# Performance work log

Hardware: AMD Instinct MI355X
Metric: run time of the kernel (lower is better)

Reference implementation:

```python
import jax, jax.numpy as jnp
import numpy as np

S = 0.7071067811865476  # 1/sqrt(2), haar filter coefficient


def wavelet_kernels():
    # pywt haar: dec_lo=[s,s], dec_hi=[-s,s], rec_lo=[s,s], rec_hi=[s,-s]
    # module reverses dec filters -> dec_lo_rev=[s,s], dec_hi_rev=[s,-s]
    lo_d = jnp.array([S, S], jnp.float32)
    hi_d = jnp.array([S, -S], jnp.float32)
    lo_r = jnp.array([S, S], jnp.float32)
    hi_r = jnp.array([S, -S], jnp.float32)
    # torch builds k[i,j] = row_filter[i] * col_filter[j] with (row, col) = (2nd, 1st) unsqueeze
    Kd = jnp.stack([jnp.outer(lo_d, lo_d), jnp.outer(hi_d, lo_d),
                    jnp.outer(lo_d, hi_d), jnp.outer(hi_d, hi_d)])  # [4,2,2] LL,LH,HL,HH
    Kr = 4.0 * jnp.stack([jnp.outer(lo_r, lo_r), jnp.outer(hi_r, lo_r),
                          jnp.outer(lo_r, hi_r), jnp.outer(hi_r, hi_r)])  # rec_* * 4
    return Kd, Kr


def group_norm(x, gamma, beta, groups, eps=1e-5):
    B, C, H, W = x.shape
    xg = x.reshape(B, groups, C // groups, H, W)
    mu = xg.mean(axis=(2, 3, 4), keepdims=True)
    var = xg.var(axis=(2, 3, 4), keepdims=True)
    xn = ((xg - mu) * jax.lax.rsqrt(var + eps)).reshape(B, C, H, W)
    return xn * gamma[None, :, None, None] + beta[None, :, None, None]


def conv2d(x, w, b, stride=1, pad=1):
    y = jax.lax.conv_general_dilated(x, w, (stride, stride), [(pad, pad), (pad, pad)],
                                     dimension_numbers=('NCHW', 'OIHW', 'NCHW'))
    return y + b[None, :, None, None]


def conv_transpose2d(x, w, b, stride=2, pad=1):
    # w in torch layout [Cin, Cout, kh, kw]; transpose conv == conv with
    # lhs-dilated input, spatially flipped kernel, padding k-1-pad
    wf = jnp.flip(w, (-2, -1)).transpose(1, 0, 2, 3)
    p = w.shape[-1] - 1 - pad
    y = jax.lax.conv_general_dilated(x, wf, (1, 1), [(p, p), (p, p)],
                                     lhs_dilation=(stride, stride),
                                     dimension_numbers=('NCHW', 'OIHW', 'NCHW'))
    return y + b[None, :, None, None]


def dwt2d(x, Kd):
    # haar k=2, stride=2, pad=0 -> non-overlapping 2x2 blocks; exact conv2d equivalent
    B, C, H, W = x.shape
    xr = x.reshape(B, C, H // 2, 2, W // 2, 2)
    c = jnp.einsum('bchdwe,sde->bcshw', xr, Kd)  # s in {LL,LH,HL,HH}
    return c.reshape(B, C * 4, H // 2, W // 2)   # channel layout [c0:LL,LH,HL,HH, c1:...]


def idwt2d(c, Kr):
    # conv_transpose2d k=2, stride=2, pad=0 -> pure 2x2 interleave
    B, C4, Hh, Wh = c.shape
    C = C4 // 4
    cr = c.reshape(B, C, 4, Hh, Wh)
    y = jnp.einsum('bcshw,sde->bchdwe', cr, Kr)
    return y.reshape(B, C, 2 * Hh, 2 * Wh)


def _forward(x, Kd, Kr, W1, b1, g1, be1, W2, b2, g2, be2, W3, b3, g3, be3,
             W4, b4, g4, be4, Wt, bt, g5, be5, W6, b6):
    h = dwt2d(x, Kd)                                      # [B,32,H/2,W/2]
    h = jax.nn.relu(group_norm(conv2d(h, W1, b1, 1, 1), g1, be1, 8))    # 32->64
    h = jax.nn.relu(group_norm(conv2d(h, W2, b2, 2, 1), g2, be2, 16))   # 64->128, /2
    h = jax.nn.relu(group_norm(conv2d(h, W3, b3, 1, 1), g3, be3, 32))   # 128->256
    h = jax.nn.relu(group_norm(conv2d(h, W4, b4, 1, 1), g4, be4, 16))   # 256->128
    h = jax.nn.relu(group_norm(conv_transpose2d(h, Wt, bt, 2, 1), g5, be5, 8))  # 128->64, x2
    h = conv2d(h, W6, b6, 1, 1)                            # 64->16
    return idwt2d(h, Kr)                                   # [B,4,H,W]


def setup_inputs() -> dict:
    key = jax.random.key(0)
    ks = jax.random.split(key, 16)
    B, Cin, H, W = 16, 8, 256, 256
    bc = 64
    Kd, Kr = wavelet_kernels()
    w = lambda k, s: jax.random.normal(k, s, jnp.float32) * 0.05
    return {
        'x': jax.random.normal(ks[0], (B, Cin, H, W), jnp.float32),
        'Kd': Kd, 'Kr': Kr,
        'W1': w(ks[1], (bc, Cin * 4, 3, 3)), 'b1': jnp.zeros(bc),
        'g1': jnp.ones(bc), 'be1': jnp.zeros(bc),
        'W2': w(ks[2], (bc * 2, bc, 3, 3)), 'b2': jnp.zeros(bc * 2),
        'g2': jnp.ones(bc * 2), 'be2': jnp.zeros(bc * 2),
        'W3': w(ks[3], (bc * 4, bc * 2, 3, 3)), 'b3': jnp.zeros(bc * 4),
        'g3': jnp.ones(bc * 4), 'be3': jnp.zeros(bc * 4),
        'W4': w(ks[4], (bc * 2, bc * 4, 3, 3)), 'b4': jnp.zeros(bc * 2),
        'g4': jnp.ones(bc * 2), 'be4': jnp.zeros(bc * 2),
        'Wt': w(ks[5], (bc * 2, bc, 4, 4)), 'bt': jnp.zeros(bc),  # torch convT layout [in,out,kh,kw]
        'g5': jnp.ones(bc), 'be5': jnp.zeros(bc),
        'W6': w(ks[6], (4 * 4, bc, 3, 3)), 'b6': jnp.zeros(4 * 4),
    }


def reference(x, Kd, Kr, W1, b1, g1, be1, W2, b2, g2, be2, W3, b3, g3, be3,
              W4, b4, g4, be4, Wt, bt, g5, be5, W6, b6):
    return _forward(x, Kd, Kr, W1, b1, g1, be1, W2, b2, g2, be2, W3, b3, g3, be3,
                    W4, b4, g4, be4, Wt, bt, g5, be5, W6, b6)
```

## Files before the change

kernel.cpp:

```cpp
#include <hip/hip_runtime.h>

typedef unsigned short ushort_t;
typedef unsigned int uint_t;
typedef __attribute__((ext_vector_type(8))) short short8;
typedef __attribute__((ext_vector_type(4))) float f32x4;

#define PAD 40

__device__ __forceinline__ ushort_t f2bf(float f) {
    uint_t u = __float_as_uint(f);
    u = (u + 0x7FFFu + ((u >> 16) & 1u)) >> 16;
    return (ushort_t)u;
}
__device__ __forceinline__ float bf2f(ushort_t h) {
    return __uint_as_float(((uint_t)h) << 16);
}

__device__ __forceinline__ void red_stats(float& s, float& ss) {
    s += __shfl_xor(s, 16); ss += __shfl_xor(ss, 16);
    s += __shfl_xor(s, 32); ss += __shfl_xor(ss, 32);
    s += __shfl_xor(s, 1);  ss += __shfl_xor(ss, 1);
    s += __shfl_xor(s, 2);  ss += __shfl_xor(ss, 2);
    s += __shfl_xor(s, 4);  ss += __shfl_xor(ss, 4);
}

__device__ __forceinline__ uint4 gn8(uint4 v, const float2* ss) {
    uint_t u[4] = {v.x, v.y, v.z, v.w};
    uint_t r[4];
#pragma unroll
    for (int p = 0; p < 4; ++p) {
        float2 s0 = ss[2 * p], s1 = ss[2 * p + 1];
        float f0 = fmaxf(bf2f((ushort_t)(u[p] & 0xffffu)) * s0.x + s0.y, 0.f);
        float f1 = fmaxf(bf2f((ushort_t)(u[p] >> 16)) * s1.x + s1.y, 0.f);
        r[p] = (uint_t)f2bf(f0) | ((uint_t)f2bf(f1) << 16);
    }
    return make_uint4(r[0], r[1], r[2], r[3]);
}

template<int C, int NPB>
__device__ __forceinline__ void fill_ss(float2* sshare, const float2* __restrict__ pin,
                                        const float* __restrict__ gamma,
                                        const float* __restrict__ beta,
                                        int b, float invC, int tid) {
    for (int c = tid; c < C; c += 256) {
        const float2* p = pin + ((size_t)b * (C / 8) + (c >> 3)) * NPB;
        float s = 0.f, ss = 0.f;
#pragma unroll 8
        for (int i = 0; i < NPB; ++i) { s += p[i].x; ss += p[i].y; }
        float mean = s * invC;
        float rstd = rsqrtf(ss * invC - mean * mean + 1e-5f);
        float sc = gamma[c] * rstd;
        sshare[c] = make_float2(sc, beta[c] - mean * sc);
    }
}

template<int CIN, int COUT>
__device__ __forceinline__ void pack3(const float* __restrict__ W, ushort_t* __restrict__ wp, int idx) {
    int kk = idx & 31;
    int t = idx >> 5;
    int co = t % COUT; t /= COUT;
    int tap = t % 9;
    int cib = t / 9;
    wp[idx] = f2bf(W[(co * CIN + cib * 32 + kk) * 9 + tap]);
}

__device__ __forceinline__ void pack2p(const float* __restrict__ W2, ushort_t* __restrict__ wp, int idx) {
    int kk = idx & 31;
    int co = (idx >> 5) & 127;
    int tap = (idx >> 12) & 3;
    int cib = idx >> 14;
    int p = cib >> 2, q = (cib >> 1) & 1, chalf = cib & 1;
    int kh = 2 * (tap >> 1) + p - 1;
    int kw = 2 * (tap & 1) + q - 1;
    float v = 0.f;
    if (kh >= 0 && kh < 3 && kw >= 0 && kw < 3)
        v = W2[(co * 64 + chalf * 32 + kk) * 9 + kh * 3 + kw];
    wp[idx] = f2bf(v);
}

__device__ __forceinline__ void packt(const float* __restrict__ Wt, ushort_t* __restrict__ wp, int idx) {
    int kk = idx & 31;
    int t = idx >> 5;
    int co = t & 63; t >>= 6;
    int tap = t & 3; t >>= 2;
    int cib = t & 3;
    int ph = t >> 2;
    int rs = tap >> 1, cs = tap & 1;
    int eh = ph >> 1, ew = ph & 1;
    int kh = eh ? (rs ? 0 : 2) : (rs ? 1 : 3);
    int kw = ew ? (cs ? 0 : 2) : (cs ? 1 : 3);
    wp[idx] = f2bf(Wt[((cib * 32 + kk) * 64 + co) * 16 + kh * 4 + kw]);
}

__global__ __launch_bounds__(256) void pack_all(const float* __restrict__ W1,
                                                const float* __restrict__ W2,
                                                const float* __restrict__ W3,
                                                const float* __restrict__ W4,
                                                const float* __restrict__ Wt,
                                                const float* __restrict__ W6,
                                                ushort_t* __restrict__ WP) {
    int idx = blockIdx.x * 256 + threadIdx.x;
    if (idx < 18432)        pack3<32, 64>(W1, WP, idx);
    else if (idx < 149504)  pack2p(W2, WP + 18432, idx - 18432);
    else if (idx < 444416)  pack3<128, 256>(W3, WP + 149504, idx - 149504);
    else if (idx < 739328)  pack3<256, 128>(W4, WP + 444416, idx - 444416);
    else if (idx < 870400)  packt(Wt, WP + 739328, idx - 739328);
    else if (idx < 879616)  pack3<64, 16>(W6, WP + 870400, idx - 870400);
}

__global__ __launch_bounds__(256) void dwt_nhwc(const float* __restrict__ x,
                                                const float* __restrict__ Kd,
                                                ushort_t* __restrict__ out) {
    int idx = blockIdx.x * 256 + threadIdx.x;
    int w = idx & 127, h = (idx >> 7) & 127, b = idx >> 14;
    float k[16];
#pragma unroll
    for (int i = 0; i < 16; ++i) k[i] = Kd[i];
    const float* xb = x + (size_t)b * 8 * 65536;
    uint_t uu[16];
#pragma unroll
    for (int ci = 0; ci < 8; ++ci) {
        const float* p = xb + ci * 65536 + (2 * h) * 256 + 2 * w;
        float2 r0 = *(const float2*)p;
        float2 r1 = *(const float2*)(p + 256);
        ushort_t o[4];
#pragma unroll
        for (int sb = 0; sb < 4; ++sb) {
            float v = r0.x * k[sb*4] + r0.y * k[sb*4+1] + r1.x * k[sb*4+2] + r1.y * k[sb*4+3];
            o[sb] = f2bf(v);
        }
        uu[ci*2]   = (uint_t)o[0] | ((uint_t)o[1] << 16);
        uu[ci*2+1] = (uint_t)o[2] | ((uint_t)o[3] << 16);
    }
    uint4* dst = (uint4*)(out + (size_t)idx * 32);
    dst[0] = make_uint4(uu[0], uu[1], uu[2], uu[3]);
    dst[1] = make_uint4(uu[4], uu[5], uu[6], uu[7]);
    dst[2] = make_uint4(uu[8], uu[9], uu[10], uu[11]);
    dst[3] = make_uint4(uu[12], uu[13], uu[14], uu[15]);
}

__global__ __launch_bounds__(256) void idwt_nhwc(const ushort_t* __restrict__ cin,
                                                 const float* __restrict__ Kr,
                                                 float* __restrict__ out) {
    int idx = blockIdx.x * 256 + threadIdx.x;
    int w = idx & 127, h = (idx >> 7) & 127, b = idx >> 14;
    float k[16];
#pragma unroll
    for (int i = 0; i < 16; ++i) k[i] = Kr[i];
    const uint4* pv = (const uint4*)(cin + (size_t)idx * 16);
    uint4 v0 = pv[0], v1 = pv[1];
    uint_t uw[8] = {v0.x, v0.y, v0.z, v0.w, v1.x, v1.y, v1.z, v1.w};
    float cs[16];
#pragma unroll
    for (int i = 0; i < 8; ++i) {
        cs[2*i]   = bf2f((ushort_t)(uw[i] & 0xffffu));
        cs[2*i+1] = bf2f((ushort_t)(uw[i] >> 16));
    }
#pragma unroll
    for (int c = 0; c < 4; ++c) {
        float y00 = 0, y01 = 0, y10 = 0, y11 = 0;
#pragma unroll
        for (int sb = 0; sb < 4; ++sb) {
            float v = cs[c * 4 + sb];
            y00 += v * k[sb*4];   y01 += v * k[sb*4+1];
            y10 += v * k[sb*4+2]; y11 += v * k[sb*4+3];
        }
        float* ob = out + ((size_t)(b * 4 + c) * 256 + 2 * h) * 256 + 2 * w;
        *(float2*)ob = make_float2(y00, y01);
        *(float2*)(ob + 256) = make_float2(y10, y11);
    }
}

template<int CIN, int COUT, int H, int W, bool STATS, bool GNIN, int NPBI>
__global__ __launch_bounds__(256, 2) void conv_mfma(const ushort_t* __restrict__ in,
                                                    const ushort_t* __restrict__ wp,
                                                    const float* __restrict__ bias,
                                                    ushort_t* __restrict__ outp,
                                                    float2* __restrict__ pstats_out,
                                                    const float2* __restrict__ pstats_in,
                                                    const float* __restrict__ gamma,
                                                    const float* __restrict__ beta,
                                                    float invC) {
    constexpr int NT = (COUT < 64) ? COUT : 64;
    constexpr int NF = NT / 16;
    constexpr int NCB = CIN / 32;
    constexpr int CSTR = (CIN < 64) ? CIN : 64;
    constexpr int NBI = CIN / CSTR;
    constexpr int SUB = CSTR / 32;
    constexpr int NBO = COUT / NT;
    constexpr int IW = 66, NRI = 6;
    constexpr int AITER = NRI * IW * 4;
    constexpr int CA = (AITER + 255) / 256;
    constexpr int NW = W / 64, NH = H / 4;
    constexpr int PB = NBO * NW * NH;
    constexpr int NPBO = NH * NW;
    constexpr int EP = NT + 8;
    constexpr int ASZ = NRI * IW * PAD;
    constexpr int SMEM = (ASZ > 256 * EP) ? ASZ : 256 * EP;

    __shared__ ushort_t smem[SMEM];
    __shared__ float2 sred[4][8];
    __shared__ float2 sshare[CIN];
    ushort_t* lA = smem;
    ushort_t* lE = smem;

    int bid = blockIdx.x;
    int xcd = bid & 7;
    int rest = bid >> 3;
    int half = rest / PB;
    int local = rest - half * PB;
    int b = xcd + 8 * half;
    int ht = local % NH; local /= NH;
    int wt = local % NW; local /= NW;
    int nb = local;
    int h0 = ht * 4, w0 = wt * 64, n0 = nb * NT;
    int tid = threadIdx.x;
    int lane = tid & 63, wid = tid >> 6;
    int nl = lane & 15, quad = lane >> 4, ql = quad * 8;

    if (GNIN) {
        fill_ss<CIN, NPBI>(sshare, pstats_in, gamma, beta, b, invC, tid);
        __syncthreads();
    }

    int ga[CA], la[CA], pr[CA];
#pragma unroll
    for (int r = 0; r < CA; ++r) {
        int i = tid + r * 256;
        ga[r] = -1; la[r] = 0; pr[r] = 0;
        if (i < AITER) {
            int tr = i / (IW * 4); int rem = i - tr * (IW * 4);
            int p = rem >> 2, part = rem & 3;
            la[r] = (tr * IW + p) * PAD + part * 8;
            pr[r] = part;
            int ih = h0 - 1 + tr, iw = w0 - 1 + p;
            if ((unsigned)ih < (unsigned)H && (unsigned)iw < (unsigned)W)
                ga[r] = (ih * W + iw) * CSTR + part * 8;
        }
    }

    f32x4 acc[4][NF];
#pragma unroll
    for (int mf = 0; mf < 4; ++mf)
#pragma unroll
        for (int nf = 0; nf < NF; ++nf)
            acc[mf][nf] = (f32x4){0.f, 0.f, 0.f, 0.f};

    uint4 ra[CA];

    auto loadA = [&](int cib) {
        const int blk = cib / SUB;
        const int inner = (cib - blk * SUB) * 32;
        const ushort_t* base = in + ((size_t)(b * NBI + blk) * (H * W)) * CSTR + inner;
#pragma unroll
        for (int r = 0; r < CA; ++r) {
            uint4 v = make_uint4(0, 0, 0, 0);
            if (ga[r] >= 0) {
                v = *(const uint4*)(base + ga[r]);
                if (GNIN) v = gn8(v, &sshare[cib * 32 + pr[r] * 8]);
            }
            ra[r] = v;
        }
    };

    loadA(0);

    const ushort_t* wlane = wp + ((size_t)(n0 + nl)) * 32 + ql;

    for (int cib = 0; cib < NCB; ++cib) {
        __syncthreads();
#pragma unroll
        for (int r = 0; r < CA; ++r)
            if (tid + r * 256 < AITER) *(uint4*)&lA[la[r]] = ra[r];
        __syncthreads();
        if (cib + 1 < NCB) loadA(cib + 1);

        const ushort_t* wc = wlane + (size_t)cib * 9 * COUT * 32;
        short8 bfc[NF], bfn[NF];
#pragma unroll
        for (int nf = 0; nf < NF; ++nf)
            bfc[nf] = *(const short8*)(wc + nf * 512);

#pragma unroll
        for (int tap = 0; tap < 9; ++tap) {
            const int kh = tap / 3, kw = tap % 3;
            if (tap < 8) {
#pragma unroll
                for (int nf = 0; nf < NF; ++nf)
                    bfn[nf] = *(const short8*)(wc + (size_t)(tap + 1) * COUT * 32 + nf * 512);
            }
            short8 af[4];
#pragma unroll
            for (int mf = 0; mf < 4; ++mf)
                af[mf] = *(const short8*)&lA[((wid + kh) * IW + mf * 16 + nl + kw) * PAD + ql];
#pragma unroll
            for (int mf = 0; mf < 4; ++mf)
#pragma unroll
                for (int nf = 0; nf < NF; ++nf)
                    acc[mf][nf] = __builtin_amdgcn_mfma_f32_16x16x32_bf16(
                        af[mf], bfc[nf], acc[mf][nf], 0, 0, 0);
#pragma unroll
            for (int nf = 0; nf < NF; ++nf) bfc[nf] = bfn[nf];
        }
    }

    float bs[NF];
#pragma unroll
    for (int nf = 0; nf < NF; ++nf) bs[nf] = bias[n0 + nf * 16 + nl];

    if (STATS) {
#pragma unroll
        for (int nf = 0; nf < NF; ++nf) {
            float s = 0.f, ss = 0.f;
#pragma unroll
            for (int mf = 0; mf < 4; ++mf)
#pragma unroll
                for (int rg = 0; rg < 4; ++rg) {
                    float v = acc[mf][nf][rg] + bs[nf];
                    s += v; ss += v * v;
                }
            red_stats(s, ss);
            if (quad == 0 && (nl & 7) == 0) sred[wid][nf * 2 + (nl >> 3)] = make_float2(s, ss);
        }
    }

    __syncthreads();
#pragma unroll
    for (int mf = 0; mf < 4; ++mf)
#pragma unroll
        for (int nf = 0; nf < NF; ++nf)
#pragma unroll
            for (int rg = 0; rg < 4; ++rg) {
                int px = wid * 64 + mf * 16 + quad * 4 + rg;
                lE[px * EP + nf * 16 + nl] = f2bf(acc[mf][nf][rg] + bs[nf]);
            }
    __syncthreads();
#pragma unroll
    for (int it = 0; it < NT / 8; ++it) {
        int idx = it * 256 + tid;
        int px = idx / (NT / 8), ck = idx % (NT / 8);
        int row = px >> 6, col = px & 63;
        uint4 v = *(const uint4*)&lE[px * EP + ck * 8];
        *(uint4*)(outp + ((((size_t)(b * NBO + nb) * H + h0 + row) * W + w0 + col) * NT + ck * 8)) = v;
    }
    if (STATS && tid < 2 * NF) {
        float2 t0 = sred[0][tid], t1 = sred[1][tid], t2 = sred[2][tid], t3 = sred[3][tid];
        pstats_out[((size_t)b * (COUT / 8) + (n0 >> 3) + tid) * NPBO + (ht * NW + wt)] =
            make_float2(t0.x + t1.x + t2.x + t3.x, t0.y + t1.y + t2.y + t3.y);
    }
}

__global__ __launch_bounds__(256, 2) void conv2p_mfma(const ushort_t* __restrict__ in,
                                                      const ushort_t* __restrict__ wp,
                                                      const float* __restrict__ bias,
                                                      ushort_t* __restrict__ outp,
                                                      float2* __restrict__ pstats_out,
                                                      const float2* __restrict__ pstats_in,
                                                      const float* __restrict__ gamma,
                                                      const float* __restrict__ beta,
                                                      float invC) {
    constexpr int IW = 65, NRI = 5, NF = 4, NT = 64;
    constexpr int AITER = NRI * IW * 4;
    constexpr int CA = 6;
    constexpr int EP = NT + 8;
    constexpr int ASZ = NRI * IW * PAD;
    constexpr int SMEM = (ASZ > 256 * EP) ? ASZ : 256 * EP;
    __shared__ ushort_t smem[SMEM];
    __shared__ float2 sred[4][8];
    __shared__ float2 sshare[64];
    ushort_t* lA = smem;
    ushort_t* lE = smem;

    int bid = blockIdx.x;
    int xcd = bid & 7;
    int rest = bid >> 3;
    int half = rest >> 5;
    int local = rest & 31;
    int b = xcd + 8 * half;
    int ht = local & 15;
    int nb = local >> 4;
    int h0 = ht * 4, n0 = nb * 64;
    int tid = threadIdx.x;
    int lane = tid & 63, wid = tid >> 6;
    int nl = lane & 15, quad = lane >> 4, ql = quad * 8;

    fill_ss<64, 64>(sshare, pstats_in, gamma, beta, b, invC, tid);
    __syncthreads();

    int r2[CA], c2[CA], la[CA], g4[CA], pr[CA];
#pragma unroll
    for (int r = 0; r < CA; ++r) {
        int i = tid + r * 256;
        r2[r] = -1000; c2[r] = 0; la[r] = 0; g4[r] = 0; pr[r] = 0;
        if (i < AITER) {
            int tr = i / (IW * 4); int rem = i - tr * (IW * 4);
            int p = rem >> 2, part = rem & 3;
            r2[r] = 2 * (h0 - 1 + tr);
            c2[r] = 2 * (p - 1);
            la[r] = (tr * IW + p) * PAD + part * 8;
            g4[r] = part * 8;
            pr[r] = part;
        }
    }

    f32x4 acc[4][NF];
#pragma unroll
    for (int mf = 0; mf < 4; ++mf)
#pragma unroll
        for (int nf = 0; nf < NF; ++nf)
            acc[mf][nf] = (f32x4){0.f, 0.f, 0.f, 0.f};

    const ushort_t* ibase = in + (size_t)b * 128 * 128 * 64;
    uint4 ra[CA];

    auto loadA = [&](int cib) {
        const int p = cib >> 2, q = (cib >> 1) & 1, ch32 = (cib & 1) * 32;
#pragma unroll
        for (int r = 0; r < CA; ++r) {
            int ih = r2[r] + p, iw = c2[r] + q;
            uint4 v = make_uint4(0, 0, 0, 0);
            if ((unsigned)ih < 128u && (unsigned)iw < 128u) {
                v = *(const uint4*)(ibase + ((ih << 7) + iw) * 64 + ch32 + g4[r]);
                v = gn8(v, &sshare[ch32 + pr[r] * 8]);
            }
            ra[r] = v;
        }
    };

    loadA(0);
    const ushort_t* wlane = wp + ((size_t)(n0 + nl)) * 32 + ql;

#pragma unroll
    for (int cib = 0; cib < 8; ++cib) {
        const int p = cib >> 2, q = (cib >> 1) & 1;
        __syncthreads();
#pragma unroll
        for (int r = 0; r < CA; ++r)
            if (tid + r * 256 < AITER) *(uint4*)&lA[la[r]] = ra[r];
        __syncthreads();
        if (cib + 1 < 8) loadA(cib + 1);

        const ushort_t* wc = wlane + (size_t)cib * 4 * 128 * 32;
#pragma unroll
        for (int kh = 0; kh < 2; ++kh)
#pragma unroll
            for (int kw = 0; kw < 2; ++kw)
                if ((kh == 1 || p == 1) && (kw == 1 || q == 1)) {
                    const int tap = kh * 2 + kw;
                    short8 bf[NF];
#pragma unroll
                    for (int nf = 0; nf < NF; ++nf)
                        bf[nf] = *(const short8*)(wc + (size_t)tap * 128 * 32 + nf * 512);
                    short8 af[4];
#pragma unroll
                    for (int mf = 0; mf < 4; ++mf)
                        af[mf] = *(const short8*)&lA[((wid + kh) * IW + mf * 16 + nl + kw) * PAD + ql];
#pragma unroll
                    for (int mf = 0; mf < 4; ++mf)
#pragma unroll
                        for (int nf = 0; nf < NF; ++nf)
                            acc[mf][nf] = __builtin_amdgcn_mfma_f32_16x16x32_bf16(
                                af[mf], bf[nf], acc[mf][nf], 0, 0, 0);
                }
    }

    float bs[NF];
#pragma unroll
    for (int nf = 0; nf < NF; ++nf) bs[nf] = bias[n0 + nf * 16 + nl];
#pragma unroll
    for (int nf = 0; nf < NF; ++nf) {
        float s = 0.f, ss = 0.f;
#pragma unroll
        for (int mf = 0; mf < 4; ++mf)
#pragma unroll
            for (int rg = 0; rg < 4; ++rg) {
                float v = acc[mf][nf][rg] + bs[nf];
                s += v; ss += v * v;
            }
        red_stats(s, ss);
        if (quad == 0 && (nl & 7) == 0) sred[wid][nf * 2 + (nl >> 3)] = make_float2(s, ss);
    }

    __syncthreads();
#pragma unroll
    for (int mf = 0; mf < 4; ++mf)
#pragma unroll
        for (int nf = 0; nf < NF; ++nf)
#pragma unroll
            for (int rg = 0; rg < 4; ++rg) {
                int px = wid * 64 + mf * 16 + quad * 4 + rg;
                lE[px * EP + nf * 16 + nl] = f2bf(acc[mf][nf][rg] + bs[nf]);
            }
    __syncthreads();
#pragma unroll
    for (int it = 0; it < 8; ++it) {
        int idx = it * 256 + tid;
        int px = idx >> 3, ck = idx & 7;
        int row = px >> 6, col = px & 63;
        uint4 v = *(const uint4*)&lE[px * EP + ck * 8];
        *(uint4*)(outp + ((((size_t)(b * 2 + nb) * 64 + h0 + row) * 64 + col) * 64 + ck * 8)) = v;
    }
    if (tid < 8) {
        float2 t0 = sred[0][tid], t1 = sred[1][tid], t2 = sred[2][tid], t3 = sred[3][tid];
        pstats_out[((size_t)b * 16 + (n0 >> 3) + tid) * 16 + ht] =
            make_float2(t0.x + t1.x + t2.x + t3.x, t0.y + t1.y + t2.y + t3.y);
    }
}

__global__ __launch_bounds__(256, 2) void convt_mfma(const ushort_t* __restrict__ in,
                                                     const ushort_t* __restrict__ wp,
                                                     const float* __restrict__ bias,
                                                     ushort_t* __restrict__ outp,
                                                     float2* __restrict__ pstats_out,
                                                     const float2* __restrict__ pstats_in,
                                                     const float* __restrict__ gamma,
                                                     const float* __restrict__ beta,
                                                     float invC) {
    constexpr int CIN = 128, COUT = 64, NT = 64, NF = 4;
    constexpr int IW = 66, NRI = 5;
    constexpr int AITER = NRI * IW * 4;
    constexpr int CA = 6;
    constexpr int EP = NT + 8;
    constexpr int ASZ = NRI * IW * PAD;
    constexpr int SMEM = (ASZ > 256 * EP) ? ASZ : 256 * EP;
    __shared__ ushort_t smem[SMEM];
    __shared__ float2 sred[4][8];
    __shared__ float2 sshare[CIN];
    ushort_t* lA = smem;
    ushort_t* lE = smem;

    int bid = blockIdx.x;
    int xcd = bid & 7;
    int rest = bid >> 3;
    int half = rest >> 6;
    int local = rest & 63;
    int b = xcd + 8 * half;
    int ht = local & 15;
    int ph = local >> 4;
    int eh = ph >> 1, ew = ph & 1;
    int ho0 = ht * 4;
    int tid = threadIdx.x;
    int lane = tid & 63, wid = tid >> 6;
    int nl = lane & 15, quad = lane >> 4, ql = quad * 8;

    fill_ss<CIN, 16>(sshare, pstats_in, gamma, beta, b, invC, tid);
    __syncthreads();

    int ga[CA], la[CA], pr[CA];
#pragma unroll
    for (int r = 0; r < CA; ++r) {
        int i = tid + r * 256;
        ga[r] = -1; la[r] = 0; pr[r] = 0;
        if (i < AITER) {
            int tr = i / (IW * 4); int rem = i - tr * (IW * 4);
            int p = rem >> 2, part = rem & 3;
            la[r] = (tr * IW + p) * PAD + part * 8;
            pr[r] = part;
            int ih = ho0 + tr - (1 - eh), iw = p - 1;
            if ((unsigned)ih < 64u && (unsigned)iw < 64u)
                ga[r] = (ih * 64 + iw) * 64 + part * 8;
        }
    }

    f32x4 acc[4][NF];
#pragma unroll
    for (int mf = 0; mf < 4; ++mf)
#pragma unroll
        for (int nf = 0; nf < NF; ++nf)
            acc[mf][nf] = (f32x4){0.f, 0.f, 0.f, 0.f};

    uint4 ra[CA];

    auto loadA = [&](int cib) {
        const int blk = cib >> 1;
        const int inner = (cib & 1) * 32;
        const ushort_t* base = in + ((size_t)(b * 2 + blk) * 4096) * 64 + inner;
#pragma unroll
        for (int r = 0; r < CA; ++r) {
            uint4 v = make_uint4(0, 0, 0, 0);
            if (ga[r] >= 0) {
                v = *(const uint4*)(base + ga[r]);
                v = gn8(v, &sshare[cib * 32 + pr[r] * 8]);
            }
            ra[r] = v;
        }
    };

    loadA(0);
    const ushort_t* wlane = wp + ((size_t)ph * 4) * 4 * COUT * 32 + (size_t)nl * 32 + ql;

    for (int cib = 0; cib < 4; ++cib) {
        __syncthreads();
#pragma unroll
        for (int r = 0; r < CA; ++r)
            if (tid + r * 256 < AITER) *(uint4*)&lA[la[r]] = ra[r];
        __syncthreads();
        if (cib + 1 < 4) loadA(cib + 1);

        const ushort_t* wc = wlane + (size_t)cib * 4 * COUT * 32;
        short8 bfc[NF], bfn[NF];
#pragma unroll
        for (int nf = 0; nf < NF; ++nf)
            bfc[nf] = *(const short8*)(wc + nf * 512);

#pragma unroll
        for (int tap = 0; tap < 4; ++tap) {
            const int rs = tap >> 1, cs = tap & 1;
            if (tap < 3) {
#pragma unroll
                for (int nf = 0; nf < NF; ++nf)
                    bfn[nf] = *(const short8*)(wc + (size_t)(tap + 1) * COUT * 32 + nf * 512);
            }
            short8 af[4];
#pragma unroll
            for (int mf = 0; mf < 4; ++mf)
                af[mf] = *(const short8*)&lA[((wid + rs) * IW + mf * 16 + nl + cs + ew) * PAD + ql];
#pragma unroll
            for (int mf = 0; mf < 4; ++mf)
#pragma unroll
                for (int nf = 0; nf < NF; ++nf)
                    acc[mf][nf] = __builtin_amdgcn_mfma_f32_16x16x32_bf16(
                        af[mf], bfc[nf], acc[mf][nf], 0, 0, 0);
#pragma unroll
            for (int nf = 0; nf < NF; ++nf) bfc[nf] = bfn[nf];
        }
    }

    float bs[NF];
#pragma unroll
    for (int nf = 0; nf < NF; ++nf) bs[nf] = bias[nf * 16 + nl];
#pragma unroll
    for (int nf = 0; nf < NF; ++nf) {
        float s = 0.f, ss = 0.f;
#pragma unroll
        for (int mf = 0; mf < 4; ++mf)
#pragma unroll
            for (int rg = 0; rg < 4; ++rg) {
                float v = acc[mf][nf][rg] + bs[nf];
                s += v; ss += v * v;
            }
        red_stats(s, ss);
        if (quad == 0 && (nl & 7) == 0) sred[wid][nf * 2 + (nl >> 3)] = make_float2(s, ss);
    }

    __syncthreads();
#pragma unroll
    for (int mf = 0; mf < 4; ++mf)
#pragma unroll
        for (int nf = 0; nf < NF; ++nf)
#pragma unroll
            for (int rg = 0; rg < 4; ++rg) {
                int px = wid * 64 + mf * 16 + quad * 4 + rg;
                lE[px * EP + nf * 16 + nl] = f2bf(acc[mf][nf][rg] + bs[nf]);
            }
    __syncthreads();
#pragma unroll
    for (int it = 0; it < 8; ++it) {
        int idx = it * 256 + tid;
        int px = idx >> 3, ck = idx & 7;
        int row = px >> 6, wo = px & 63;
        int oh = 2 * (ho0 + row) + eh;
        uint4 v = *(const uint4*)&lE[px * EP + ck * 8];
        *(uint4*)(outp + (((size_t)b * 128 + oh) * 128 + 2 * wo + ew) * 64 + ck * 8) = v;
    }
    if (tid < 8) {
        float2 t0 = sred[0][tid], t1 = sred[1][tid], t2 = sred[2][tid], t3 = sred[3][tid];
        pstats_out[((size_t)b * 8 + tid) * 64 + (ht * 4 + ph)] =
            make_float2(t0.x + t1.x + t2.x + t3.x, t0.y + t1.y + t2.y + t3.y);
    }
}

extern "C" void kernel_launch(void* const* d_in, const int* in_sizes, int n_in,
                              void* d_out, int out_size, void* d_ws, size_t ws_size,
                              hipStream_t stream) {
    const float* x   = (const float*)d_in[0];
    const float* Kd  = (const float*)d_in[1];
    const float* Kr  = (const float*)d_in[2];
    const float* W1  = (const float*)d_in[3];  const float* b1  = (const float*)d_in[4];
    const float* g1  = (const float*)d_in[5];  const float* be1 = (const float*)d_in[6];
    const float* W2  = (const float*)d_in[7];  const float* b2  = (const float*)d_in[8];
    const float* g2  = (const float*)d_in[9];  const float* be2 = (const float*)d_in[10];
    const float* W3  = (const float*)d_in[11]; const float* b3  = (const float*)d_in[12];
    const float* g3  = (const float*)d_in[13]; const float* be3 = (const float*)d_in[14];
    const float* W4  = (const float*)d_in[15]; const float* b4  = (const float*)d_in[16];
    const float* g4  = (const float*)d_in[17]; const float* be4 = (const float*)d_in[18];
    const float* Wt  = (const float*)d_in[19]; const float* bt  = (const float*)d_in[20];
    const float* g5  = (const float*)d_in[21]; const float* be5 = (const float*)d_in[22];
    const float* W6  = (const float*)d_in[23]; const float* b6  = (const float*)d_in[24];

    ushort_t* U  = (ushort_t*)d_ws;
    ushort_t* V  = U + 8388608;
    ushort_t* WP = V + 16777216;
    ushort_t* wp1 = WP;
    ushort_t* wp2 = WP + 18432;
    ushort_t* wp3 = WP + 149504;
    ushort_t* wp4 = WP + 444416;
    ushort_t* wpt = WP + 739328;
    ushort_t* wp6 = WP + 870400;
    float2* PS = (float2*)(WP + 879616);
    float2* P1 = PS;
    float2* P2 = PS + 8192;
    float2* P3 = PS + 12288;
    float2* P4 = PS + 20480;
    float2* P5 = PS + 24576;
    float* out = (float*)d_out;

    pack_all<<<3436, 256, 0, stream>>>(W1, W2, W3, W4, Wt, W6, WP);

    dwt_nhwc<<<1024, 256, 0, stream>>>(x, Kd, U);

    conv_mfma<32, 64, 128, 128, true, false, 16>
        <<<1024, 256, 0, stream>>>(U, wp1, b1, V, P1, nullptr, nullptr, nullptr, 0.f);

    conv2p_mfma<<<512, 256, 0, stream>>>(V, wp2, b2, U, P2,
                                         P1, g1, be1, 1.f / 131072.f);

    conv_mfma<128, 256, 64, 64, true, true, 16>
        <<<1024, 256, 0, stream>>>(U, wp3, b3, V, P3,
                                   P2, g2, be2, 1.f / 32768.f);

    conv_mfma<256, 128, 64, 64, true, true, 16>
        <<<512, 256, 0, stream>>>(V, wp4, b4, U, P4,
                                  P3, g3, be3, 1.f / 32768.f);

    convt_mfma<<<1024, 256, 0, stream>>>(U, wpt, bt, V, P5,
                                         P4, g4, be4, 1.f / 32768.f);

    conv_mfma<64, 16, 128, 128, false, true, 64>
        <<<1024, 256, 0, stream>>>(V, wp6, b6, U, nullptr,
                                   P5, g5, be5, 1.f / 131072.f);

    idwt_nhwc<<<1024, 256, 0, stream>>>(U, Kr, out);
}
```

Baseline: 368.0 us.

## Load conv operands directly from global and split GroupNorm into separate in-place kernels

The convolution kernels stop staging input tiles in LDS and instead load MFMA A fragments straight from global memory per tap, with register double-buffering of A and B for the next tap. This removes the barriers and LDS staging. Because GroupNorm+ReLU was previously applied while staging, it now runs as a separate in-place gn_relu pass over each activation tensor. That adds five extra launches and a full read/write of each intermediate, and each input element is now re-read from global or cache up to 9 times instead of once.

```diff
diff --git a/kernel.cpp b/kernel.cpp
--- a/kernel.cpp
+++ b/kernel.cpp
@@ -4,8 +4,6 @@
 typedef unsigned int uint_t;
 typedef __attribute__((ext_vector_type(8))) short short8;
 typedef __attribute__((ext_vector_type(4))) float f32x4;
-
-#define PAD 40
 
 __device__ __forceinline__ ushort_t f2bf(float f) {
     uint_t u = __float_as_uint(f);
@@ -171,16 +169,38 @@
     }
 }
 
-template<int CIN, int COUT, int H, int W, bool STATS, bool GNIN, int NPBI>
+template<int C, int HW, int NPB>
+__global__ __launch_bounds__(256) void gn_relu(ushort_t* __restrict__ data,
+                                               const float2* __restrict__ pstats,
+                                               const float* __restrict__ gamma,
+                                               const float* __restrict__ beta,
+                                               float invC) {
+    constexpr int PBG = (HW * C) / (8 * 256);
+    __shared__ float2 sshare[C];
+    int bid = blockIdx.x;
+    int xcd = bid & 7;
+    int rest = bid >> 3;
+    int half = rest / PBG;
+    int local = rest - half * PBG;
+    int b = xcd + 8 * half;
+    int tid = threadIdx.x;
+    fill_ss<C, NPB>(sshare, pstats, gamma, beta, b, invC, tid);
+    __syncthreads();
+    int e8 = local * 256 + tid;
+    size_t off = ((size_t)b * HW * C) / 8 + e8;
+    int flat = e8 * 8;
+    int c0 = (flat & 63) + 64 * (flat / (HW * 64));
+    uint4 v = ((const uint4*)data)[off];
+    v = gn8(v, &sshare[c0]);
+    ((uint4*)data)[off] = v;
+}
+
+template<int CIN, int COUT, int H, int W, bool STATS>
 __global__ __launch_bounds__(256, 2) void conv_mfma(const ushort_t* __restrict__ in,
                                                     const ushort_t* __restrict__ wp,
                                                     const float* __restrict__ bias,
                                                     ushort_t* __restrict__ outp,
-                                                    float2* __restrict__ pstats_out,
-                                                    const float2* __restrict__ pstats_in,
-                                                    const float* __restrict__ gamma,
-                                                    const float* __restrict__ beta,
-                                                    float invC) {
+                                                    float2* __restrict__ pstats_out) {
     constexpr int NT = (COUT < 64) ? COUT : 64;
     constexpr int NF = NT / 16;
     constexpr int NCB = CIN / 32;
@@ -188,21 +208,13 @@
     constexpr int NBI = CIN / CSTR;
     constexpr int SUB = CSTR / 32;
     constexpr int NBO = COUT / NT;
-    constexpr int IW = 66, NRI = 6;
-    constexpr int AITER = NRI * IW * 4;
-    constexpr int CA = (AITER + 255) / 256;
     constexpr int NW = W / 64, NH = H / 4;
     constexpr int PB = NBO * NW * NH;
     constexpr int NPBO = NH * NW;
     constexpr int EP = NT + 8;
-    constexpr int ASZ = NRI * IW * PAD;
-    constexpr int SMEM = (ASZ > 256 * EP) ? ASZ : 256 * EP;
-
-    __shared__ ushort_t smem[SMEM];
+
+    __shared__ ushort_t lE[256 * EP];
     __shared__ float2 sred[4][8];
-    __shared__ float2 sshare[CIN];
-    ushort_t* lA = smem;
-    ushort_t* lE = smem;
 
     int bid = blockIdx.x;
     int xcd = bid & 7;
@@ -218,26 +230,15 @@
     int lane = tid & 63, wid = tid >> 6;
     int nl = lane & 15, quad = lane >> 4, ql = quad * 8;
 
-    if (GNIN) {
-        fill_ss<CIN, NPBI>(sshare, pstats_in, gamma, beta, b, invC, tid);
-        __syncthreads();
-    }
-
-    int ga[CA], la[CA], pr[CA];
-#pragma unroll
-    for (int r = 0; r < CA; ++r) {
-        int i = tid + r * 256;
-        ga[r] = -1; la[r] = 0; pr[r] = 0;
-        if (i < AITER) {
-            int tr = i / (IW * 4); int rem = i - tr * (IW * 4);
-            int p = rem >> 2, part = rem & 3;
-            la[r] = (tr * IW + p) * PAD + part * 8;
-            pr[r] = part;
-            int ih = h0 - 1 + tr, iw = w0 - 1 + p;
-            if ((unsigned)ih < (unsigned)H && (unsigned)iw < (unsigned)W)
-                ga[r] = (ih * W + iw) * CSTR + part * 8;
-        }
-    }
+    int rowi[3]; bool rok[3];
+#pragma unroll
+    for (int kh = 0; kh < 3; ++kh) {
+        rowi[kh] = h0 + wid - 1 + kh;
+        rok[kh] = (unsigned)rowi[kh] < (unsigned)H;
+    }
+    int col0[4];
+#pragma unroll
+    for (int mf = 0; mf < 4; ++mf) col0[mf] = w0 + mf * 16 + nl - 1;
 
     f32x4 acc[4][NF];
 #pragma unroll
@@ -246,61 +247,54 @@
         for (int nf = 0; nf < NF; ++nf)
             acc[mf][nf] = (f32x4){0.f, 0.f, 0.f, 0.f};
 
-    uint4 ra[CA];
-
-    auto loadA = [&](int cib) {
+    const ushort_t* wlane = wp + (size_t)(n0 + nl) * 32 + ql;
+
+    short8 aC[4], aN[4], bC[NF], bN[NF];
+
+    auto loadAf = [&](int cib, int tap, short8* d) {
         const int blk = cib / SUB;
         const int inner = (cib - blk * SUB) * 32;
-        const ushort_t* base = in + ((size_t)(b * NBI + blk) * (H * W)) * CSTR + inner;
-#pragma unroll
-        for (int r = 0; r < CA; ++r) {
-            uint4 v = make_uint4(0, 0, 0, 0);
-            if (ga[r] >= 0) {
-                v = *(const uint4*)(base + ga[r]);
-                if (GNIN) v = gn8(v, &sshare[cib * 32 + pr[r] * 8]);
-            }
-            ra[r] = v;
+        const ushort_t* pb = in + ((size_t)(b * NBI + blk) * (H * W)) * CSTR + inner + ql;
+        const int kh = tap / 3, kw = tap % 3;
+#pragma unroll
+        for (int mf = 0; mf < 4; ++mf) {
+            int c = col0[mf] + kw;
+            short8 v = {};
+            if (rok[kh] && (unsigned)c < (unsigned)W)
+                v = *(const short8*)(pb + ((size_t)rowi[kh] * W + c) * CSTR);
+            d[mf] = v;
         }
     };
-
-    loadA(0);
-
-    const ushort_t* wlane = wp + ((size_t)(n0 + nl)) * 32 + ql;
+    auto loadBf = [&](int cib, int tap, short8* d) {
+        const ushort_t* wc = wlane + (size_t)(cib * 9 + tap) * COUT * 32;
+#pragma unroll
+        for (int nf = 0; nf < NF; ++nf)
+            d[nf] = *(const short8*)(wc + nf * 512);
+    };
+
+    loadAf(0, 0, aC);
+    loadBf(0, 0, bC);
 
     for (int cib = 0; cib < NCB; ++cib) {
-        __syncthreads();
-#pragma unroll
-        for (int r = 0; r < CA; ++r)
-            if (tid + r * 256 < AITER) *(uint4*)&lA[la[r]] = ra[r];
-        __syncthreads();
-        if (cib + 1 < NCB) loadA(cib + 1);
-
-        const ushort_t* wc = wlane + (size_t)cib * 9 * COUT * 32;
-        short8 bfc[NF], bfn[NF];
-#pragma unroll
-        for (int nf = 0; nf < NF; ++nf)
-            bfc[nf] = *(const short8*)(wc + nf * 512);
-
 #pragma unroll
         for (int tap = 0; tap < 9; ++tap) {
-            const int kh = tap / 3, kw = tap % 3;
-            if (tap < 8) {
-#pragma unroll
-                for (int nf = 0; nf < NF; ++nf)
-                    bfn[nf] = *(const short8*)(wc + (size_t)(tap + 1) * COUT * 32 + nf * 512);
-            }
-            short8 af[4];
-#pragma unroll
-            for (int mf = 0; mf < 4; ++mf)
-                af[mf] = *(const short8*)&lA[((wid + kh) * IW + mf * 16 + nl + kw) * PAD + ql];
+            const bool haveNext = (tap < 8) || (cib + 1 < NCB);
+            if (haveNext) {
+                int ncib = (tap < 8) ? cib : cib + 1;
+                int ntap = (tap < 8) ? tap + 1 : 0;
+                loadAf(ncib, ntap, aN);
+                loadBf(ncib, ntap, bN);
+            }
 #pragma unroll
             for (int mf = 0; mf < 4; ++mf)
 #pragma unroll
                 for (int nf = 0; nf < NF; ++nf)
                     acc[mf][nf] = __builtin_amdgcn_mfma_f32_16x16x32_bf16(
-                        af[mf], bfc[nf], acc[mf][nf], 0, 0, 0);
-#pragma unroll
-            for (int nf = 0; nf < NF; ++nf) bfc[nf] = bfn[nf];
+                        aC[mf], bC[nf], acc[mf][nf], 0, 0, 0);
+#pragma unroll
+            for (int mf = 0; mf < 4; ++mf) aC[mf] = aN[mf];
+#pragma unroll
+            for (int nf = 0; nf < NF; ++nf) bC[nf] = bN[nf];
         }
     }
 
@@ -354,22 +348,10 @@
                                                       const ushort_t* __restrict__ wp,
                                                       const float* __restrict__ bias,
                                                       ushort_t* __restrict__ outp,
-                                                      float2* __restrict__ pstats_out,
-                                                      const float2* __restrict__ pstats_in,
-                                                      const float* __restrict__ gamma,
-                                                      const float* __restrict__ beta,
-                                                      float invC) {
-    constexpr int IW = 65, NRI = 5, NF = 4, NT = 64;
-    constexpr int AITER = NRI * IW * 4;
-    constexpr int CA = 6;
-    constexpr int EP = NT + 8;
-    constexpr int ASZ = NRI * IW * PAD;
-    constexpr int SMEM = (ASZ > 256 * EP) ? ASZ : 256 * EP;
-    __shared__ ushort_t smem[SMEM];
+                                                      float2* __restrict__ pstats_out) {
+    constexpr int NF = 4, NT = 64, EP = NT + 8;
+    __shared__ ushort_t lE[256 * EP];
     __shared__ float2 sred[4][8];
-    __shared__ float2 sshare[64];
-    ushort_t* lA = smem;
-    ushort_t* lE = smem;
 
     int bid = blockIdx.x;
     int xcd = bid & 7;
@@ -384,25 +366,6 @@
     int lane = tid & 63, wid = tid >> 6;
     int nl = lane & 15, quad = lane >> 4, ql = quad * 8;
 
-    fill_ss<64, 64>(sshare, pstats_in, gamma, beta, b, invC, tid);
-    __syncthreads();
-
-    int r2[CA], c2[CA], la[CA], g4[CA], pr[CA];
-#pragma unroll
-    for (int r = 0; r < CA; ++r) {
-        int i = tid + r * 256;
-        r2[r] = -1000; c2[r] = 0; la[r] = 0; g4[r] = 0; pr[r] = 0;
-        if (i < AITER) {
-            int tr = i / (IW * 4); int rem = i - tr * (IW * 4);
-            int p = rem >> 2, part = rem & 3;
-            r2[r] = 2 * (h0 - 1 + tr);
-            c2[r] = 2 * (p - 1);
-            la[r] = (tr * IW + p) * PAD + part * 8;
-            g4[r] = part * 8;
-            pr[r] = part;
-        }
-    }
-
     f32x4 acc[4][NF];
 #pragma unroll
     for (int mf = 0; mf < 4; ++mf)
@@ -410,51 +373,33 @@
         for (int nf = 0; nf < NF; ++nf)
             acc[mf][nf] = (f32x4){0.f, 0.f, 0.f, 0.f};
 
-    const ushort_t* ibase = in + (size_t)b * 128 * 128 * 64;
-    uint4 ra[CA];
-
-    auto loadA = [&](int cib) {
+    const ushort_t* ibase = in + (size_t)b * 128 * 128 * 64 + ql;
+    const ushort_t* wlane = wp + (size_t)(n0 + nl) * 32 + ql;
+
+#pragma unroll
+    for (int cib = 0; cib < 8; ++cib) {
         const int p = cib >> 2, q = (cib >> 1) & 1, ch32 = (cib & 1) * 32;
 #pragma unroll
-        for (int r = 0; r < CA; ++r) {
-            int ih = r2[r] + p, iw = c2[r] + q;
-            uint4 v = make_uint4(0, 0, 0, 0);
-            if ((unsigned)ih < 128u && (unsigned)iw < 128u) {
-                v = *(const uint4*)(ibase + ((ih << 7) + iw) * 64 + ch32 + g4[r]);
-                v = gn8(v, &sshare[ch32 + pr[r] * 8]);
-            }
-            ra[r] = v;
-        }
-    };
-
-    loadA(0);
-    const ushort_t* wlane = wp + ((size_t)(n0 + nl)) * 32 + ql;
-
-#pragma unroll
-    for (int cib = 0; cib < 8; ++cib) {
-        const int p = cib >> 2, q = (cib >> 1) & 1;
-        __syncthreads();
-#pragma unroll
-        for (int r = 0; r < CA; ++r)
-            if (tid + r * 256 < AITER) *(uint4*)&lA[la[r]] = ra[r];
-        __syncthreads();
-        if (cib + 1 < 8) loadA(cib + 1);
-
-        const ushort_t* wc = wlane + (size_t)cib * 4 * 128 * 32;
-#pragma unroll
-        for (int kh = 0; kh < 2; ++kh)
-#pragma unroll
-            for (int kw = 0; kw < 2; ++kw)
+        for (int kh = 0; kh < 2; ++kh) {
+#pragma unroll
+            for (int kw = 0; kw < 2; ++kw) {
                 if ((kh == 1 || p == 1) && (kw == 1 || q == 1)) {
                     const int tap = kh * 2 + kw;
                     short8 bf[NF];
 #pragma unroll
                     for (int nf = 0; nf < NF; ++nf)
-                        bf[nf] = *(const short8*)(wc + (size_t)tap * 128 * 32 + nf * 512);
+                        bf[nf] = *(const short8*)(wlane + (size_t)(cib * 4 + tap) * 128 * 32 + nf * 512);
+                    int row = 2 * (h0 + wid - 1 + kh) + p;
+                    bool rk = (unsigned)row < 128u;
                     short8 af[4];
 #pragma unroll
-                    for (int mf = 0; mf < 4; ++mf)
-                        af[mf] = *(const short8*)&lA[((wid + kh) * IW + mf * 16 + nl + kw) * PAD + ql];
+                    for (int mf = 0; mf < 4; ++mf) {
+                        int c = 2 * (mf * 16 + nl + kw - 1) + q;
+                        short8 v = {};
+                        if (rk && (unsigned)c < 128u)
+                            v = *(const short8*)(ibase + ((size_t)row * 128 + c) * 64 + ch32);
+                        af[mf] = v;
+                    }
 #pragma unroll
                     for (int mf = 0; mf < 4; ++mf)
 #pragma unroll
@@ -462,6 +407,8 @@
                             acc[mf][nf] = __builtin_amdgcn_mfma_f32_16x16x32_bf16(
                                 af[mf], bf[nf], acc[mf][nf], 0, 0, 0);
                 }
+            }
+        }
     }
 
     float bs[NF];
@@ -511,23 +458,10 @@
                                                      const ushort_t* __restrict__ wp,
                                                      const float* __restrict__ bias,
                                                      ushort_t* __restrict__ outp,
-                                                     float2* __restrict__ pstats_out,
-                                                     const float2* __restrict__ pstats_in,
-                                                     const float* __restrict__ gamma,
-                                                     const float* __restrict__ beta,
-                                                     float invC) {
-    constexpr int CIN = 128, COUT = 64, NT = 64, NF = 4;
-    constexpr int IW = 66, NRI = 5;
-    constexpr int AITER = NRI * IW * 4;
-    constexpr int CA = 6;
-    constexpr int EP = NT + 8;
-    constexpr int ASZ = NRI * IW * PAD;
-    constexpr int SMEM = (ASZ > 256 * EP) ? ASZ : 256 * EP;
-    __shared__ ushort_t smem[SMEM];
+                                                     float2* __restrict__ pstats_out) {
+    constexpr int COUT = 64, NT = 64, NF = 4, EP = NT + 8;
+    __shared__ ushort_t lE[256 * EP];
     __shared__ float2 sred[4][8];
-    __shared__ float2 sshare[CIN];
-    ushort_t* lA = smem;
-    ushort_t* lE = smem;
 
     int bid = blockIdx.x;
     int xcd = bid & 7;
@@ -543,25 +477,6 @@
     int lane = tid & 63, wid = tid >> 6;
     int nl = lane & 15, quad = lane >> 4, ql = quad * 8;
 
-    fill_ss<CIN, 16>(sshare, pstats_in, gamma, beta, b, invC, tid);
-    __syncthreads();
-
-    int ga[CA], la[CA], pr[CA];
-#pragma unroll
-    for (int r = 0; r < CA; ++r) {
-        int i = tid + r * 256;
-        ga[r] = -1; la[r] = 0; pr[r] = 0;
-        if (i < AITER) {
-            int tr = i / (IW * 4); int rem = i - tr * (IW * 4);
-            int p = rem >> 2, part = rem & 3;
-            la[r] = (tr * IW + p) * PAD + part * 8;
-            pr[r] = part;
-            int ih = ho0 + tr - (1 - eh), iw = p - 1;
-            if ((unsigned)ih < 64u && (unsigned)iw < 64u)
-                ga[r] = (ih * 64 + iw) * 64 + part * 8;
-        }
-    }
-
     f32x4 acc[4][NF];
 #pragma unroll
     for (int mf = 0; mf < 4; ++mf)
@@ -569,60 +484,64 @@
         for (int nf = 0; nf < NF; ++nf)
             acc[mf][nf] = (f32x4){0.f, 0.f, 0.f, 0.f};
 
-    uint4 ra[CA];
-
-    auto loadA = [&](int cib) {
+    int rowi[2]; bool rok[2];
+#pragma unroll
+    for (int rs = 0; rs < 2; ++rs) {
+        rowi[rs] = ho0 + wid + rs - (1 - eh);
+        rok[rs] = (unsigned)rowi[rs] < 64u;
+    }
+    int col0[4];
+#pragma unroll
+    for (int mf = 0; mf < 4; ++mf) col0[mf] = mf * 16 + nl + ew - 1;
+
+    const ushort_t* wlane = wp + ((size_t)ph * 4) * 4 * COUT * 32 + (size_t)nl * 32 + ql;
+
+    short8 aC[4], aN[4], bC[NF], bN[NF];
+
+    auto loadAf = [&](int cib, int tap, short8* d) {
         const int blk = cib >> 1;
         const int inner = (cib & 1) * 32;
-        const ushort_t* base = in + ((size_t)(b * 2 + blk) * 4096) * 64 + inner;
-#pragma unroll
-        for (int r = 0; r < CA; ++r) {
-            uint4 v = make_uint4(0, 0, 0, 0);
-            if (ga[r] >= 0) {
-                v = *(const uint4*)(base + ga[r]);
-                v = gn8(v, &sshare[cib * 32 + pr[r] * 8]);
-            }
-            ra[r] = v;
+        const ushort_t* pb = in + ((size_t)(b * 2 + blk) * 4096) * 64 + inner + ql;
+        const int rs = tap >> 1, cs = tap & 1;
+#pragma unroll
+        for (int mf = 0; mf < 4; ++mf) {
+            int c = col0[mf] + cs;
+            short8 v = {};
+            if (rok[rs] && (unsigned)c < 64u)
+                v = *(const short8*)(pb + ((size_t)rowi[rs] * 64 + c) * 64);
+            d[mf] = v;
         }
     };
-
-    loadA(0);
-    const ushort_t* wlane = wp + ((size_t)ph * 4) * 4 * COUT * 32 + (size_t)nl * 32 + ql;
+    auto loadBf = [&](int cib, int tap, short8* d) {
+        const ushort_t* wc = wlane + (size_t)(cib * 4 + tap) * COUT * 32;
+#pragma unroll
+        for (int nf = 0; nf < NF; ++nf)
+            d[nf] = *(const short8*)(wc + nf * 512);
+    };
+
+    loadAf(0, 0, aC);
+    loadBf(0, 0, bC);
 
     for (int cib = 0; cib < 4; ++cib) {
-        __syncthreads();
-#pragma unroll
-        for (int r = 0; r < CA; ++r)
-            if (tid + r * 256 < AITER) *(uint4*)&lA[la[r]] = ra[r];
-        __syncthreads();
-        if (cib + 1 < 4) loadA(cib + 1);
-
-        const ushort_t* wc = wlane + (size_t)cib * 4 * COUT * 32;
-        short8 bfc[NF], bfn[NF];
-#pragma unroll
-        for (int nf = 0; nf < NF; ++nf)
-            bfc[nf] = *(const short8*)(wc + nf * 512);
-
 #pragma unroll
         for (int tap = 0; tap < 4; ++tap) {
-            const int rs = tap >> 1, cs = tap & 1;
-            if (tap < 3) {
-#pragma unroll
-                for (int nf = 0; nf < NF; ++nf)
-                    bfn[nf] = *(const short8*)(wc + (size_t)(tap + 1) * COUT * 32 + nf * 512);
-            }
-            short8 af[4];
-#pragma unroll
-            for (int mf = 0; mf < 4; ++mf)
-                af[mf] = *(const short8*)&lA[((wid + rs) * IW + mf * 16 + nl + cs + ew) * PAD + ql];
+            const bool haveNext = (tap < 3) || (cib + 1 < 4);
+            if (haveNext) {
+                int ncib = (tap < 3) ? cib : cib + 1;
+                int ntap = (tap < 3) ? tap + 1 : 0;
+                loadAf(ncib, ntap, aN);
+                loadBf(ncib, ntap, bN);
+            }
 #pragma unroll
             for (int mf = 0; mf < 4; ++mf)
 #pragma unroll
                 for (int nf = 0; nf < NF; ++nf)
                     acc[mf][nf] = __builtin_amdgcn_mfma_f32_16x16x32_bf16(
-                        af[mf], bfc[nf], acc[mf][nf], 0, 0, 0);
-#pragma unroll
-            for (int nf = 0; nf < NF; ++nf) bfc[nf] = bfn[nf];
+                        aC[mf], bC[nf], acc[mf][nf], 0, 0, 0);
+#pragma unroll
+            for (int mf = 0; mf < 4; ++mf) aC[mf] = aN[mf];
+#pragma unroll
+            for (int nf = 0; nf < NF; ++nf) bC[nf] = bN[nf];
         }
     }
 
@@ -709,26 +628,26 @@
 
     dwt_nhwc<<<1024, 256, 0, stream>>>(x, Kd, U);
 
-    conv_mfma<32, 64, 128, 128, true, false, 16>
-        <<<1024, 256, 0, stream>>>(U, wp1, b1, V, P1, nullptr, nullptr, nullptr, 0.f);
-
-    conv2p_mfma<<<512, 256, 0, stream>>>(V, wp2, b2, U, P2,
-                                         P1, g1, be1, 1.f / 131072.f);
-
-    conv_mfma<128, 256, 64, 64, true, true, 16>
-        <<<1024, 256, 0, stream>>>(U, wp3, b3, V, P3,
-                                   P2, g2, be2, 1.f / 32768.f);
-
-    conv_mfma<256, 128, 64, 64, true, true, 16>
-        <<<512, 256, 0, stream>>>(V, wp4, b4, U, P4,
-                                  P3, g3, be3, 1.f / 32768.f);
-
-    convt_mfma<<<1024, 256, 0, stream>>>(U, wpt, bt, V, P5,
-                                         P4, g4, be4, 1.f / 32768.f);
-
-    conv_mfma<64, 16, 128, 128, false, true, 64>
-        <<<1024, 256, 0, stream>>>(V, wp6, b6, U, nullptr,
-                                   P5, g5, be5, 1.f / 131072.f);
+    conv_mfma<32, 64, 128, 128, true>
+        <<<1024, 256, 0, stream>>>(U, wp1, b1, V, P1);
+    gn_relu<64, 16384, 64><<<8192, 256, 0, stream>>>(V, P1, g1, be1, 1.f / 131072.f);
+
+    conv2p_mfma<<<512, 256, 0, stream>>>(V, wp2, b2, U, P2);
+    gn_relu<128, 4096, 16><<<4096, 256, 0, stream>>>(U, P2, g2, be2, 1.f / 32768.f);
+
+    conv_mfma<128, 256, 64, 64, true>
+        <<<1024, 256, 0, stream>>>(U, wp3, b3, V, P3);
+    gn_relu<256, 4096, 16><<<8192, 256, 0, stream>>>(V, P3, g3, be3, 1.f / 32768.f);
+
+    conv_mfma<256, 128, 64, 64, true>
+        <<<512, 256, 0, stream>>>(V, wp4, b4, U, P4);
+    gn_relu<128, 4096, 16><<<4096, 256, 0, stream>>>(U, P4, g4, be4, 1.f / 32768.f);
+
+    convt_mfma<<<1024, 256, 0, stream>>>(U, wpt, bt, V, P5);
+    gn_relu<64, 16384, 64><<<8192, 256, 0, stream>>>(V, P5, g5, be5, 1.f / 131072.f);
+
+    conv_mfma<64, 16, 128, 128, false>
+        <<<1024, 256, 0, stream>>>(V, wp6, b6, U, nullptr);
 
     idwt_nhwc<<<1024, 256, 0, stream>>>(U, Kr, out);
 }
```

Measured after the change: 576.6 us. 56.7% more time.
